# Optimization experiments

Hardware: AMD Instinct MI355X
Metric: run time of the kernel (lower is better)

The kernel has to match this reference:

```python
import jax, jax.numpy as jnp
import numpy as np

N_NODES = 100000
N_REL = 500
DIM = 200
N_EDGES = 200000
T_STEPS = 3
EPS = 1e-12


def _l2norm(x):
    # F.normalize(x): L2 along last dim with eps clamp
    n = jnp.sqrt(jnp.sum(x * x, axis=-1, keepdims=True))
    return x / jnp.maximum(n, EPS)


def _rgcn_layer(h, r, src, rel, dst, W_msg, W_loop):
    # UnionRGCN layer: msg = (h[src] + r[rel]) @ W_msg, mean-aggregated at dst,
    # plus self-loop transform. No activation (active=False), dropout=0.
    msg = (h[src] + r[rel]) @ W_msg                      # [E, D]
    deg = jax.ops.segment_sum(jnp.ones((src.shape[0],), h.dtype), dst,
                              num_segments=N_NODES)       # [N]
    agg = jax.ops.segment_sum(msg, dst, num_segments=N_NODES)
    agg = agg / jnp.maximum(deg, 1.0)[:, None]
    return agg + h @ W_loop


def setup_inputs() -> dict:
    key = jax.random.key(0)
    ks = jax.random.split(key, 10)
    edge_list = []
    for t in range(T_STEPS):
        kt = jax.random.fold_in(ks[0], t)
        k1, k2, k3 = jax.random.split(kt, 3)
        src = jax.random.randint(k1, (N_EDGES,), 0, N_NODES)
        rel = jax.random.randint(k2, (N_EDGES,), 0, N_REL)
        dst = jax.random.randint(k3, (N_EDGES,), 0, N_NODES)
        edge_list.append(jnp.stack([src, rel, dst], axis=1))
    edges = jnp.stack(edge_list)  # [T, E, 3]
    s = 1.0 / np.sqrt(DIM)
    return {
        "edges": edges,
        "entity_embed": jax.random.normal(ks[1], (N_NODES, DIM), jnp.float32),
        "relation_embed": jax.random.normal(ks[2], (N_REL, DIM), jnp.float32),
        "W_msg1": jax.random.normal(ks[3], (DIM, DIM), jnp.float32) * s,
        "W_loop1": jax.random.normal(ks[4], (DIM, DIM), jnp.float32) * s,
        "W_msg2": jax.random.normal(ks[5], (DIM, DIM), jnp.float32) * s,
        "W_loop2": jax.random.normal(ks[6], (DIM, DIM), jnp.float32) * s,
        "time_gate_weight": jax.random.normal(ks[7], (DIM, DIM), jnp.float32) * s * np.sqrt(2.0),
        "time_gate_bias": jnp.zeros((DIM,), jnp.float32),
    }


def reference(edges, entity_embed, relation_embed, W_msg1, W_loop1, W_msg2,
              W_loop2, time_gate_weight, time_gate_bias):
    h = _l2norm(entity_embed)
    r = _l2norm(relation_embed)
    for t in range(T_STEPS):  # small fixed temporal loop, as in source
        src, rel, dst = edges[t, :, 0], edges[t, :, 1], edges[t, :, 2]
        cur = _rgcn_layer(h, r, src, rel, dst, W_msg1, W_loop1)
        cur = _rgcn_layer(cur, r, src, rel, dst, W_msg2, W_loop2)
        cur = _l2norm(cur)
        gate = jax.nn.sigmoid(h @ time_gate_weight + time_gate_bias)
        h = _l2norm(gate * cur + (1.0 - gate) * h)
    return h
```

## Files before the change

kernel.cpp:

```cpp
#include <hip/hip_runtime.h>
#include <math.h>

#define DIMN   200
#define NNODES 100000
#define NREL   500
#define NEDGES 200000
#define TSTEPS 3
#define KSTEPS 7
#define NB16   16
#define WPK_ELEMS (KSTEPS * NB16 * 64 * 8)
#define SCAN_B 1024
#define NBN    6252
#define FRAG_STRIDE 3584

typedef float  v4f  __attribute__((ext_vector_type(4)));
typedef __bf16 v8bf __attribute__((ext_vector_type(8)));

__device__ __forceinline__ size_t frag_chunk(int nb, int c, int r) {
    return (size_t)(nb * KSTEPS + (c >> 2)) * 512 + (size_t)((c & 3) * 128 + r * 8);
}

__launch_bounds__(256)
__global__ void l2norm_pro(const float* __restrict__ in, __bf16* __restrict__ outR,
                           __bf16* __restrict__ outF, int nrows)
{
    int idx  = blockIdx.x * 256 + threadIdx.x;
    int node = idx >> 5;
    int ch   = idx & 31;
    if (node >= nrows) return;
    float v[8] = {};
    if (ch < 25) {
        const float4* p = (const float4*)(in + (size_t)node * DIMN + ch * 8);
        float4 f0 = p[0], f1 = p[1];
        v[0]=f0.x; v[1]=f0.y; v[2]=f0.z; v[3]=f0.w;
        v[4]=f1.x; v[5]=f1.y; v[6]=f1.z; v[7]=f1.w;
    }
    float ss = 0.0f;
    #pragma unroll
    for (int k = 0; k < 8; ++k) ss += v[k] * v[k];
    #pragma unroll
    for (int off = 16; off; off >>= 1) ss += __shfl_xor(ss, off, 64);
    float s = 1.0f / fmaxf(sqrtf(ss), 1e-12f);
    #pragma unroll
    for (int k = 0; k < 8; ++k) v[k] *= s;
    if (ch < 25) {
        v8bf o;
        #pragma unroll
        for (int k = 0; k < 8; ++k) o[k] = (__bf16)v[k];
        *(v8bf*)(outR + (size_t)node * DIMN + ch * 8) = o;
    }
    if (outF && ch < 28) {
        v8bf o;
        #pragma unroll
        for (int k = 0; k < 8; ++k) o[k] = (ch < 25) ? (__bf16)v[k] : (__bf16)0.0f;
        *(v8bf*)(outF + frag_chunk(node >> 4, ch, node & 15)) = o;
    }
}

__launch_bounds__(256)
__global__ void edge_hist3(const int* __restrict__ edges, int* __restrict__ counts)
{
    int e = blockIdx.x * 256 + threadIdx.x;
    if (e < TSTEPS * NEDGES) {
        int t = e / NEDGES;
        atomicAdd(&counts[t * NNODES + edges[(size_t)e * 3 + 2]], 1);
    }
}

__launch_bounds__(SCAN_B)
__global__ void scan1(const int* __restrict__ counts, int* __restrict__ tmp,
                      int* __restrict__ bsum, int n)
{
    __shared__ int sh[SCAN_B];
    int i = blockIdx.x * SCAN_B + threadIdx.x;
    int v = (i < n) ? counts[i] : 0;
    sh[threadIdx.x] = v;
    __syncthreads();
    for (int off = 1; off < SCAN_B; off <<= 1) {
        int t = (threadIdx.x >= off) ? sh[threadIdx.x - off] : 0;
        __syncthreads();
        sh[threadIdx.x] += t;
        __syncthreads();
    }
    if (i < n) tmp[i] = sh[threadIdx.x];
    if (threadIdx.x == SCAN_B - 1) bsum[blockIdx.x] = sh[threadIdx.x];
}

__launch_bounds__(SCAN_B)
__global__ void scan2(int* __restrict__ bsum, int nb)
{
    __shared__ int sh[SCAN_B];
    int v = (threadIdx.x < nb) ? bsum[threadIdx.x] : 0;
    sh[threadIdx.x] = v;
    __syncthreads();
    for (int off = 1; off < SCAN_B; off <<= 1) {
        int t = (threadIdx.x >= off) ? sh[threadIdx.x - off] : 0;
        __syncthreads();
        sh[threadIdx.x] += t;
        __syncthreads();
    }
    if (threadIdx.x < nb) bsum[threadIdx.x] = sh[threadIdx.x] - v;
}

__launch_bounds__(SCAN_B)
__global__ void scan3(const int* __restrict__ tmp, const int* __restrict__ bsum,
                      int* __restrict__ offs, int n)
{
    int i = blockIdx.x * SCAN_B + threadIdx.x;
    if (i < n) offs[i + 1] = tmp[i] + bsum[blockIdx.x];
    if (i == 0) offs[0] = 0;
}

__launch_bounds__(256)
__global__ void edge_fill3(const int* __restrict__ edges, const int* __restrict__ offs,
                           int* __restrict__ cursor, int2* __restrict__ sorted)
{
    int e = blockIdx.x * 256 + threadIdx.x;
    if (e >= TSTEPS * NEDGES) return;
    int t = e / NEDGES;
    int s = edges[(size_t)e * 3 + 0];
    int r = edges[(size_t)e * 3 + 1];
    int d = edges[(size_t)e * 3 + 2];
    int sn = t * NNODES + d;
    int p = offs[sn] + atomicAdd(&cursor[sn], 1);
    sorted[p] = make_int2(s, r);
}

__launch_bounds__(256)
__global__ void agg_S(const int* __restrict__ offs, const int2* __restrict__ sorted,
                      const __bf16* __restrict__ XR, const __bf16* __restrict__ RnR,
                      __bf16* __restrict__ SF, int nnodes)
{
    int wave = (int)((blockIdx.x * blockDim.x + threadIdx.x) >> 6);
    int lane = threadIdx.x & 63;
    if (wave >= nnodes) return;
    int beg = offs[wave], end = offs[wave + 1];
    int ch = lane & 31;
    bool act = ch < 25;

    float acc[8] = {};
    for (int e = beg; e < end; ++e) {
        int2 sr = sorted[e];
        const __bf16* base = (lane < 32) ? (XR + (size_t)sr.x * DIMN)
                                         : (RnR + (size_t)sr.y * DIMN);
        v8bf v = {};
        if (act) v = *(const v8bf*)(base + ch * 8);
        #pragma unroll
        for (int k = 0; k < 8; ++k) acc[k] += (float)v[k];
    }
    #pragma unroll
    for (int k = 0; k < 8; ++k) acc[k] += __shfl_xor(acc[k], 32, 64);

    float rdeg = 1.0f / fmaxf((float)(end - beg), 1.0f);
    if (lane < 32 && ch < 28) {
        v8bf o;
        #pragma unroll
        for (int k = 0; k < 8; ++k) o[k] = act ? (__bf16)(acc[k] * rdeg) : (__bf16)0.0f;
        *(v8bf*)(SF + frag_chunk(wave >> 4, ch, wave & 15)) = o;
    }
}

__launch_bounds__(256)
__global__ void pack_w(const float* __restrict__ W0, const float* __restrict__ W1,
                       const float* __restrict__ W2, const float* __restrict__ W3,
                       const float* __restrict__ W4, __bf16* __restrict__ out)
{
    int id = blockIdx.x * 256 + threadIdx.x;
    const int nchunk = KSTEPS * NB16 * 64;
    if (id >= 5 * nchunk) return;
    int wi = id / nchunk;
    int c  = id % nchunk;
    const float* W = wi == 0 ? W0 : wi == 1 ? W1 : wi == 2 ? W2 : wi == 3 ? W3 : W4;
    int s    = c >> 10;
    int nb   = (c & 1023) >> 6;
    int lane = c & 63;
    int kbase = s * 32 + (lane >> 4) * 8;
    int n     = nb * 16 + (lane & 15);
    __bf16* dst = out + (size_t)wi * WPK_ELEMS + (size_t)c * 8;
    #pragma unroll
    for (int j = 0; j < 8; ++j) {
        int k = kbase + j;
        float v = (k < DIMN && n < DIMN) ? W[k * DIMN + n] : 0.0f;
        dst[j] = (__bf16)v;
    }
}

__launch_bounds__(512)
__global__ void gemm_dual(const __bf16* __restrict__ A1, const __bf16* __restrict__ W1,
                          const __bf16* __restrict__ A2, const __bf16* __restrict__ W2,
                          __bf16* __restrict__ OutR, __bf16* __restrict__ OutF, int M)
{
    const int tid  = threadIdx.x;
    const int w    = tid >> 6;
    const int lane = tid & 63;
    const int rlo  = lane & 15;
    const int g    = lane >> 4;
    const int nb0  = blockIdx.x * 4;
    const int bm   = blockIdx.x * 64;

    __shared__ __bf16 T[64][264];

    v4f acc[4][2];
    #pragma unroll
    for (int mi = 0; mi < 4; ++mi)
        #pragma unroll
        for (int ni = 0; ni < 2; ++ni)
            acc[mi][ni] = (v4f){0.f, 0.f, 0.f, 0.f};

    const __bf16* w1b = W1 + (size_t)(w * 2 * 64 + lane) * 8;
    const __bf16* w2b = W2 + (size_t)(w * 2 * 64 + lane) * 8;

    #pragma unroll
    for (int s = 0; s < KSTEPS; ++s) {
        v8bf b1[2], b2[2];
        #pragma unroll
        for (int ni = 0; ni < 2; ++ni) {
            size_t bo = ((size_t)s * NB16 * 64 + ni * 64) * 8;
            b1[ni] = *(const v8bf*)(w1b + bo);
            b2[ni] = *(const v8bf*)(w2b + bo);
        }
        #pragma unroll
        for (int mi = 0; mi < 4; ++mi) {
            size_t aoff = (size_t)((nb0 + mi) * KSTEPS + s) * 512 + lane * 8;
            v8bf a1 = *(const v8bf*)(A1 + aoff);
            v8bf a2 = *(const v8bf*)(A2 + aoff);
            #pragma unroll
            for (int ni = 0; ni < 2; ++ni)
                acc[mi][ni] = __builtin_amdgcn_mfma_f32_16x16x32_bf16(a1, b1[ni], acc[mi][ni], 0, 0, 0);
            #pragma unroll
            for (int ni = 0; ni < 2; ++ni)
                acc[mi][ni] = __builtin_amdgcn_mfma_f32_16x16x32_bf16(a2, b2[ni], acc[mi][ni], 0, 0, 0);
        }
    }

    #pragma unroll
    for (int mi = 0; mi < 4; ++mi)
        #pragma unroll
        for (int reg = 0; reg < 4; ++reg)
            #pragma unroll
            for (int ni = 0; ni < 2; ++ni)
                T[mi * 16 + g * 4 + reg][w * 32 + ni * 16 + rlo] = (__bf16)acc[mi][ni][reg];
    __syncthreads();

    #pragma unroll
    for (int j = 0; j < 4; ++j) {
        int it = tid + j * 512;
        if (it < 1792) {
            int slot = it & 63;
            int q = it >> 6;
            int s = q % 7, nb = q / 7;
            *(v8bf*)(OutF + (size_t)((nb0 + nb) * KSTEPS + s) * 512 + slot * 8) =
                *(const v8bf*)&T[nb * 16 + (slot & 15)][s * 32 + (slot >> 4) * 8];
        }
    }
    #pragma unroll
    for (int j = 0; j < 4; ++j) {
        int it = tid + j * 512;
        if (it < 1600) {
            int row = it / 25, ch = it - row * 25;
            int gr = bm + row;
            if (gr < M)
                *(v8bf*)(OutR + (size_t)gr * DIMN + ch * 8) = *(const v8bf*)&T[row][ch * 8];
        }
    }
}

__launch_bounds__(512)
__global__ void gemm_mega(const __bf16* __restrict__ A1, const __bf16* __restrict__ W1,
                          const __bf16* __restrict__ A2, const __bf16* __restrict__ W2,
                          const __bf16* __restrict__ A3, const __bf16* __restrict__ W3,
                          const float* __restrict__ Bias,
                          __bf16* __restrict__ HR, __bf16* __restrict__ HF,
                          float* __restrict__ DoutF, int M, int finalStep)
{
    const int tid  = threadIdx.x;
    const int w    = tid >> 6;
    const int lane = tid & 63;
    const int rlo  = lane & 15;
    const int g    = lane >> 4;
    const int nb0  = blockIdx.x * 2;
    const int bm   = blockIdx.x * 32;

    __shared__ __bf16 T[32][264];
    __shared__ float  rsq1[32][8];
    __shared__ float  rsq2[32][8];

    v4f acc1[2][2], acc2[2][2];
    #pragma unroll
    for (int mi = 0; mi < 2; ++mi)
        #pragma unroll
        for (int ni = 0; ni < 2; ++ni) {
            acc1[mi][ni] = (v4f){0.f, 0.f, 0.f, 0.f};
            acc2[mi][ni] = (v4f){0.f, 0.f, 0.f, 0.f};
        }

    const __bf16* w1b = W1 + (size_t)(w * 2 * 64 + lane) * 8;
    const __bf16* w2b = W2 + (size_t)(w * 2 * 64 + lane) * 8;
    const __bf16* w3b = W3 + (size_t)(w * 2 * 64 + lane) * 8;

    for (int s = 0; s < KSTEPS; ++s) {
        v8bf b1[2], b2[2], b3[2];
        #pragma unroll
        for (int ni = 0; ni < 2; ++ni) {
            size_t bo = ((size_t)s * NB16 * 64 + ni * 64) * 8;
            b1[ni] = *(const v8bf*)(w1b + bo);
            b2[ni] = *(const v8bf*)(w2b + bo);
            b3[ni] = *(const v8bf*)(w3b + bo);
        }
        #pragma unroll
        for (int mi = 0; mi < 2; ++mi) {
            size_t aoff = (size_t)((nb0 + mi) * KSTEPS + s) * 512 + lane * 8;
            v8bf a1 = *(const v8bf*)(A1 + aoff);
            v8bf a2 = *(const v8bf*)(A2 + aoff);
            v8bf a3 = *(const v8bf*)(A3 + aoff);
            #pragma unroll
            for (int ni = 0; ni < 2; ++ni)
                acc1[mi][ni] = __builtin_amdgcn_mfma_f32_16x16x32_bf16(a1, b1[ni], acc1[mi][ni], 0, 0, 0);
            #pragma unroll
            for (int ni = 0; ni < 2; ++ni)
                acc1[mi][ni] = __builtin_amdgcn_mfma_f32_16x16x32_bf16(a2, b2[ni], acc1[mi][ni], 0, 0, 0);
            #pragma unroll
            for (int ni = 0; ni < 2; ++ni)
                acc2[mi][ni] = __builtin_amdgcn_mfma_f32_16x16x32_bf16(a3, b3[ni], acc2[mi][ni], 0, 0, 0);
        }
    }

    #pragma unroll
    for (int mi = 0; mi < 2; ++mi)
        #pragma unroll
        for (int reg = 0; reg < 4; ++reg) {
            float ss = 0.0f;
            #pragma unroll
            for (int ni = 0; ni < 2; ++ni) ss += acc1[mi][ni][reg] * acc1[mi][ni][reg];
            ss += __shfl_xor(ss, 1, 64);
            ss += __shfl_xor(ss, 2, 64);
            ss += __shfl_xor(ss, 4, 64);
            ss += __shfl_xor(ss, 8, 64);
            if (rlo == 0) rsq1[mi * 16 + g * 4 + reg][w] = ss;
        }
    #pragma unroll
    for (int j = 0; j < 2; ++j) {
        int it = tid + j * 512;
        if (it < 800) {
            int row = it / 25, ch = it - row * 25;
            int gr = bm + row;
            v8bf hv = {};
            if (gr < M) hv = *(const v8bf*)(HR + (size_t)gr * DIMN + ch * 8);
            *(v8bf*)&T[row][ch * 8] = hv;
        }
    }
    __syncthreads();

    #pragma unroll
    for (int mi = 0; mi < 2; ++mi)
        #pragma unroll
        for (int reg = 0; reg < 4; ++reg) {
            int rl = mi * 16 + g * 4 + reg;
            float tot = rsq1[rl][0] + rsq1[rl][1] + rsq1[rl][2] + rsq1[rl][3]
                      + rsq1[rl][4] + rsq1[rl][5] + rsq1[rl][6] + rsq1[rl][7];
            float sc1 = 1.0f / fmaxf(sqrtf(tot), 1e-12f);
            float ss = 0.0f;
            #pragma unroll
            for (int ni = 0; ni < 2; ++ni) {
                int c = w * 32 + ni * 16 + rlo;
                float v = 0.0f;
                if (c < DIMN) {
                    float cur = acc1[mi][ni][reg] * sc1;
                    float gg  = 1.0f / (1.0f + __expf(-(acc2[mi][ni][reg] + Bias[c])));
                    float hh  = (float)T[rl][c];
                    v = gg * cur + (1.0f - gg) * hh;
                }
                acc1[mi][ni][reg] = v;
                ss += v * v;
            }
            ss += __shfl_xor(ss, 1, 64);
            ss += __shfl_xor(ss, 2, 64);
            ss += __shfl_xor(ss, 4, 64);
            ss += __shfl_xor(ss, 8, 64);
            if (rlo == 0) rsq2[rl][w] = ss;
        }
    __syncthreads();

    #pragma unroll
    for (int mi = 0; mi < 2; ++mi)
        #pragma unroll
        for (int reg = 0; reg < 4; ++reg) {
            int rl = mi * 16 + g * 4 + reg;
            float tot = rsq2[rl][0] + rsq2[rl][1] + rsq2[rl][2] + rsq2[rl][3]
                      + rsq2[rl][4] + rsq2[rl][5] + rsq2[rl][6] + rsq2[rl][7];
            float sc2 = 1.0f / fmaxf(sqrtf(tot), 1e-12f);
            #pragma unroll
            for (int ni = 0; ni < 2; ++ni) {
                int c = w * 32 + ni * 16 + rlo;
                T[rl][c] = (__bf16)(acc1[mi][ni][reg] * sc2);
            }
        }
    __syncthreads();

    if (!finalStep) {
        #pragma unroll
        for (int j = 0; j < 2; ++j) {
            int it = tid + j * 512;
            if (it < 800) {
                int row = it / 25, ch = it - row * 25;
                int gr = bm + row;
                if (gr < M)
                    *(v8bf*)(HR + (size_t)gr * DIMN + ch * 8) = *(const v8bf*)&T[row][ch * 8];
            }
        }
        #pragma unroll
        for (int j = 0; j < 2; ++j) {
            int it = tid + j * 512;
            if (it < 896) {
                int slot = it & 63;
                int q = it >> 6;
                int s = q % 7, nb = q / 7;
                *(v8bf*)(HF + (size_t)((nb0 + nb) * KSTEPS + s) * 512 + slot * 8) =
                    *(const v8bf*)&T[nb * 16 + (slot & 15)][s * 32 + (slot >> 4) * 8];
            }
        }
    } else {
        #pragma unroll
        for (int j = 0; j < 2; ++j) {
            int it = tid + j * 512;
            if (it < 800) {
                int row = it / 25, ch = it - row * 25;
                int gr = bm + row;
                if (gr < M) {
                    v8bf o = *(const v8bf*)&T[row][ch * 8];
                    float4* q0 = (float4*)(DoutF + (size_t)gr * DIMN + ch * 8);
                    q0[0] = make_float4((float)o[0], (float)o[1], (float)o[2], (float)o[3]);
                    q0[1] = make_float4((float)o[4], (float)o[5], (float)o[6], (float)o[7]);
                }
            }
        }
    }
}

extern "C" void kernel_launch(void* const* d_in, const int* in_sizes, int n_in,
                              void* d_out, int out_size, void* d_ws, size_t ws_size,
                              hipStream_t stream)
{
    const int*   edges = (const int*)  d_in[0];
    const float* ent   = (const float*)d_in[1];
    const float* relE  = (const float*)d_in[2];
    const float* Wm1   = (const float*)d_in[3];
    const float* Wl1   = (const float*)d_in[4];
    const float* Wm2   = (const float*)d_in[5];
    const float* Wl2   = (const float*)d_in[6];
    const float* Wtg   = (const float*)d_in[7];
    const float* bias  = (const float*)d_in[8];
    float* Dout = (float*)d_out;

    const size_t NM    = (size_t)NNODES * DIMN;
    const size_t FRAGN = (size_t)NBN * FRAG_STRIDE;

    __bf16* hR   = (__bf16*)d_ws;
    __bf16* hF   = hR + NM;
    __bf16* SF   = hF + FRAGN;
    __bf16* BR   = SF + FRAGN;
    __bf16* BF   = BR + NM;
    __bf16* RnR  = BF + FRAGN;
    __bf16* Wpk  = RnR + (size_t)NREL * DIMN;
    __bf16* pWm1 = Wpk + 0 * (size_t)WPK_ELEMS;
    __bf16* pWl1 = Wpk + 1 * (size_t)WPK_ELEMS;
    __bf16* pWm2 = Wpk + 2 * (size_t)WPK_ELEMS;
    __bf16* pWl2 = Wpk + 3 * (size_t)WPK_ELEMS;
    __bf16* pWtg = Wpk + 4 * (size_t)WPK_ELEMS;
    int*  counts = (int*)(Wpk + 5 * (size_t)WPK_ELEMS);
    int*  cursor = counts + TSTEPS * NNODES;
    int2* sorted = (int2*)(cursor + TSTEPS * NNODES);
    int*  offs   = (int*)(sorted + TSTEPS * NEDGES);
    int*  bsum   = offs + (TSTEPS * NNODES + 1);
    int*  stmp   = bsum + SCAN_B;

    dim3 blk(256);
    const int GD = (NNODES + 63) / 64;
    const int GM = (NNODES + 31) / 32;
    dim3 ngrid32((NNODES * 32 + 255) / 256);
    dim3 rgrid32((NREL * 32 + 255) / 256);
    dim3 agrid((NNODES + 3) / 4);
    dim3 egrid3((TSTEPS * NEDGES + 255) / 256);
    const int NTOT = TSTEPS * NNODES;
    const int NSB  = (NTOT + SCAN_B - 1) / SCAN_B;

    pack_w<<<dim3((5 * KSTEPS * NB16 * 64 + 255) / 256), blk, 0, stream>>>(Wm1, Wl1, Wm2, Wl2, Wtg, Wpk);
    l2norm_pro<<<ngrid32, blk, 0, stream>>>(ent, hR, hF, NNODES);
    l2norm_pro<<<rgrid32, blk, 0, stream>>>(relE, RnR, nullptr, NREL);

    hipMemsetAsync(counts, 0, 2 * NTOT * sizeof(int), stream);
    edge_hist3<<<egrid3, blk, 0, stream>>>(edges, counts);
    scan1<<<NSB, SCAN_B, 0, stream>>>(counts, stmp, bsum, NTOT);
    scan2<<<1, SCAN_B, 0, stream>>>(bsum, NSB);
    scan3<<<NSB, SCAN_B, 0, stream>>>(stmp, bsum, offs, NTOT);
    edge_fill3<<<egrid3, blk, 0, stream>>>(edges, offs, cursor, sorted);

    for (int t = 0; t < 3; ++t) {
        const int* offsT = offs + (size_t)t * NNODES;
        agg_S<<<agrid, blk, 0, stream>>>(offsT, sorted, hR, RnR, SF, NNODES);
        gemm_dual<<<GD, dim3(512), 0, stream>>>(SF, pWm1, hF, pWl1, BR, BF, NNODES);
        agg_S<<<agrid, blk, 0, stream>>>(offsT, sorted, BR, RnR, SF, NNODES);
        gemm_mega<<<GM, dim3(512), 0, stream>>>(SF, pWm2, BF, pWl2, hF, pWtg, bias,
                                                hR, hF, Dout, NNODES, (t == 2) ? 1 : 0);
    }
}
```

Measured before the change: 967.3 us.

## Replace dual row/fragment buffers with single padded row-major bf16 layout

Activations were kept in two copies, a row-major buffer for gathers and an MFMA fragment-packed buffer for GEMMs. They now use one row-major buffer padded to a stride of 224. The GEMMs read A operands directly with per-row pointers, and the weight packing is reordered so each lane's K steps are contiguous. This removes the duplicate fragment writes in every producer kernel and shrinks the workspace. In exchange the GEMM A loads are less coalesced than the fragment-contiguous layout, and the gathers read a padded stride.

```diff
diff --git a/kernel.cpp b/kernel.cpp
--- a/kernel.cpp
+++ b/kernel.cpp
@@ -1,28 +1,23 @@
 #include <hip/hip_runtime.h>
 #include <math.h>
 
-#define DIMN   200
-#define NNODES 100000
-#define NREL   500
-#define NEDGES 200000
-#define TSTEPS 3
-#define KSTEPS 7
-#define NB16   16
+#define DIMN    200
+#define RSTRIDE 224
+#define NNODES  100000
+#define NREL    500
+#define NEDGES  200000
+#define TSTEPS  3
+#define KSTEPS  7
+#define NB16    16
 #define WPK_ELEMS (KSTEPS * NB16 * 64 * 8)
-#define SCAN_B 1024
-#define NBN    6252
-#define FRAG_STRIDE 3584
+#define SCAN_B  1024
 
 typedef float  v4f  __attribute__((ext_vector_type(4)));
 typedef __bf16 v8bf __attribute__((ext_vector_type(8)));
 
-__device__ __forceinline__ size_t frag_chunk(int nb, int c, int r) {
-    return (size_t)(nb * KSTEPS + (c >> 2)) * 512 + (size_t)((c & 3) * 128 + r * 8);
-}
 
 __launch_bounds__(256)
-__global__ void l2norm_pro(const float* __restrict__ in, __bf16* __restrict__ outR,
-                           __bf16* __restrict__ outF, int nrows)
+__global__ void l2norm_pro(const float* __restrict__ in, __bf16* __restrict__ out, int nrows)
 {
     int idx  = blockIdx.x * 256 + threadIdx.x;
     int node = idx >> 5;
@@ -41,19 +36,11 @@
     #pragma unroll
     for (int off = 16; off; off >>= 1) ss += __shfl_xor(ss, off, 64);
     float s = 1.0f / fmaxf(sqrtf(ss), 1e-12f);
-    #pragma unroll
-    for (int k = 0; k < 8; ++k) v[k] *= s;
-    if (ch < 25) {
+    if (ch < 28) {
         v8bf o;
         #pragma unroll
-        for (int k = 0; k < 8; ++k) o[k] = (__bf16)v[k];
-        *(v8bf*)(outR + (size_t)node * DIMN + ch * 8) = o;
-    }
-    if (outF && ch < 28) {
-        v8bf o;
-        #pragma unroll
-        for (int k = 0; k < 8; ++k) o[k] = (ch < 25) ? (__bf16)v[k] : (__bf16)0.0f;
-        *(v8bf*)(outF + frag_chunk(node >> 4, ch, node & 15)) = o;
+        for (int k = 0; k < 8; ++k) o[k] = (ch < 25) ? (__bf16)(v[k] * s) : (__bf16)0.0f;
+        *(v8bf*)(out + (size_t)node * RSTRIDE + ch * 8) = o;
     }
 }
 
@@ -129,7 +116,7 @@
 __launch_bounds__(256)
 __global__ void agg_S(const int* __restrict__ offs, const int2* __restrict__ sorted,
                       const __bf16* __restrict__ XR, const __bf16* __restrict__ RnR,
-                      __bf16* __restrict__ SF, int nnodes)
+                      __bf16* __restrict__ SR, int nnodes)
 {
     int wave = (int)((blockIdx.x * blockDim.x + threadIdx.x) >> 6);
     int lane = threadIdx.x & 63;
@@ -141,8 +128,8 @@
     float acc[8] = {};
     for (int e = beg; e < end; ++e) {
         int2 sr = sorted[e];
-        const __bf16* base = (lane < 32) ? (XR + (size_t)sr.x * DIMN)
-                                         : (RnR + (size_t)sr.y * DIMN);
+        const __bf16* base = (lane < 32) ? (XR + (size_t)sr.x * RSTRIDE)
+                                         : (RnR + (size_t)sr.y * RSTRIDE);
         v8bf v = {};
         if (act) v = *(const v8bf*)(base + ch * 8);
         #pragma unroll
@@ -156,7 +143,7 @@
         v8bf o;
         #pragma unroll
         for (int k = 0; k < 8; ++k) o[k] = act ? (__bf16)(acc[k] * rdeg) : (__bf16)0.0f;
-        *(v8bf*)(SF + frag_chunk(wave >> 4, ch, wave & 15)) = o;
+        *(v8bf*)(SR + (size_t)wave * RSTRIDE + ch * 8) = o;
     }
 }
 
@@ -171,9 +158,10 @@
     int wi = id / nchunk;
     int c  = id % nchunk;
     const float* W = wi == 0 ? W0 : wi == 1 ? W1 : wi == 2 ? W2 : wi == 3 ? W3 : W4;
-    int s    = c >> 10;
-    int nb   = (c & 1023) >> 6;
-    int lane = c & 63;
+    int nb   = c / 448;
+    int rem  = c - nb * 448;
+    int lane = rem / 7;
+    int s    = rem - lane * 7;
     int kbase = s * 32 + (lane >> 4) * 8;
     int n     = nb * 16 + (lane & 15);
     __bf16* dst = out + (size_t)wi * WPK_ELEMS + (size_t)c * 8;
@@ -188,14 +176,13 @@
 __launch_bounds__(512)
 __global__ void gemm_dual(const __bf16* __restrict__ A1, const __bf16* __restrict__ W1,
                           const __bf16* __restrict__ A2, const __bf16* __restrict__ W2,
-                          __bf16* __restrict__ OutR, __bf16* __restrict__ OutF, int M)
+                          __bf16* __restrict__ OutR, int M)
 {
     const int tid  = threadIdx.x;
     const int w    = tid >> 6;
     const int lane = tid & 63;
     const int rlo  = lane & 15;
-    const int g    = lane >> 4;
-    const int nb0  = blockIdx.x * 4;
+    const int g8   = lane >> 4;
     const int bm   = blockIdx.x * 64;
 
     __shared__ __bf16 T[64][264];
@@ -207,23 +194,36 @@
         for (int ni = 0; ni < 2; ++ni)
             acc[mi][ni] = (v4f){0.f, 0.f, 0.f, 0.f};
 
-    const __bf16* w1b = W1 + (size_t)(w * 2 * 64 + lane) * 8;
-    const __bf16* w2b = W2 + (size_t)(w * 2 * 64 + lane) * 8;
+    const __bf16* a1p[4];
+    const __bf16* a2p[4];
+    #pragma unroll
+    for (int mi = 0; mi < 4; ++mi) {
+        int rr = bm + mi * 16 + rlo;
+        if (rr >= M) rr = M - 1;
+        a1p[mi] = A1 + (size_t)rr * RSTRIDE + g8 * 8;
+        a2p[mi] = A2 + (size_t)rr * RSTRIDE + g8 * 8;
+    }
+    const __bf16* b1p[2];
+    const __bf16* b2p[2];
+    #pragma unroll
+    for (int ni = 0; ni < 2; ++ni) {
+        size_t bo = ((size_t)(w * 2 + ni) * 448 + lane * 7) * 8;
+        b1p[ni] = W1 + bo;
+        b2p[ni] = W2 + bo;
+    }
 
     #pragma unroll
     for (int s = 0; s < KSTEPS; ++s) {
         v8bf b1[2], b2[2];
         #pragma unroll
         for (int ni = 0; ni < 2; ++ni) {
-            size_t bo = ((size_t)s * NB16 * 64 + ni * 64) * 8;
-            b1[ni] = *(const v8bf*)(w1b + bo);
-            b2[ni] = *(const v8bf*)(w2b + bo);
+            b1[ni] = *(const v8bf*)(b1p[ni] + s * 8);
+            b2[ni] = *(const v8bf*)(b2p[ni] + s * 8);
         }
         #pragma unroll
         for (int mi = 0; mi < 4; ++mi) {
-            size_t aoff = (size_t)((nb0 + mi) * KSTEPS + s) * 512 + lane * 8;
-            v8bf a1 = *(const v8bf*)(A1 + aoff);
-            v8bf a2 = *(const v8bf*)(A2 + aoff);
+            v8bf a1 = *(const v8bf*)(a1p[mi] + s * 32);
+            v8bf a2 = *(const v8bf*)(a2p[mi] + s * 32);
             #pragma unroll
             for (int ni = 0; ni < 2; ++ni)
                 acc[mi][ni] = __builtin_amdgcn_mfma_f32_16x16x32_bf16(a1, b1[ni], acc[mi][ni], 0, 0, 0);
@@ -239,28 +239,17 @@
         for (int reg = 0; reg < 4; ++reg)
             #pragma unroll
             for (int ni = 0; ni < 2; ++ni)
-                T[mi * 16 + g * 4 + reg][w * 32 + ni * 16 + rlo] = (__bf16)acc[mi][ni][reg];
+                T[mi * 16 + g8 * 4 + reg][w * 32 + ni * 16 + rlo] = (__bf16)acc[mi][ni][reg];
     __syncthreads();
 
     #pragma unroll
     for (int j = 0; j < 4; ++j) {
         int it = tid + j * 512;
         if (it < 1792) {
-            int slot = it & 63;
-            int q = it >> 6;
-            int s = q % 7, nb = q / 7;
-            *(v8bf*)(OutF + (size_t)((nb0 + nb) * KSTEPS + s) * 512 + slot * 8) =
-                *(const v8bf*)&T[nb * 16 + (slot & 15)][s * 32 + (slot >> 4) * 8];
-        }
-    }
-    #pragma unroll
-    for (int j = 0; j < 4; ++j) {
-        int it = tid + j * 512;
-        if (it < 1600) {
-            int row = it / 25, ch = it - row * 25;
+            int row = it / 28, ch = it - row * 28;
             int gr = bm + row;
             if (gr < M)
-                *(v8bf*)(OutR + (size_t)gr * DIMN + ch * 8) = *(const v8bf*)&T[row][ch * 8];
+                *(v8bf*)(OutR + (size_t)gr * RSTRIDE + ch * 8) = *(const v8bf*)&T[row][ch * 8];
         }
     }
 }
@@ -268,17 +257,15 @@
 __launch_bounds__(512)
 __global__ void gemm_mega(const __bf16* __restrict__ A1, const __bf16* __restrict__ W1,
                           const __bf16* __restrict__ A2, const __bf16* __restrict__ W2,
-                          const __bf16* __restrict__ A3, const __bf16* __restrict__ W3,
+                          __bf16* __restrict__ HR, const __bf16* __restrict__ W3,
                           const float* __restrict__ Bias,
-                          __bf16* __restrict__ HR, __bf16* __restrict__ HF,
                           float* __restrict__ DoutF, int M, int finalStep)
 {
     const int tid  = threadIdx.x;
     const int w    = tid >> 6;
     const int lane = tid & 63;
     const int rlo  = lane & 15;
-    const int g    = lane >> 4;
-    const int nb0  = blockIdx.x * 2;
+    const int g8   = lane >> 4;
     const int bm   = blockIdx.x * 32;
 
     __shared__ __bf16 T[32][264];
@@ -294,25 +281,42 @@
             acc2[mi][ni] = (v4f){0.f, 0.f, 0.f, 0.f};
         }
 
-    const __bf16* w1b = W1 + (size_t)(w * 2 * 64 + lane) * 8;
-    const __bf16* w2b = W2 + (size_t)(w * 2 * 64 + lane) * 8;
-    const __bf16* w3b = W3 + (size_t)(w * 2 * 64 + lane) * 8;
-
+    const __bf16* a1p[2];
+    const __bf16* a2p[2];
+    const __bf16* a3p[2];
+    #pragma unroll
+    for (int mi = 0; mi < 2; ++mi) {
+        int rr = bm + mi * 16 + rlo;
+        if (rr >= M) rr = M - 1;
+        a1p[mi] = A1 + (size_t)rr * RSTRIDE + g8 * 8;
+        a2p[mi] = A2 + (size_t)rr * RSTRIDE + g8 * 8;
+        a3p[mi] = HR + (size_t)rr * RSTRIDE + g8 * 8;
+    }
+    const __bf16* b1p[2];
+    const __bf16* b2p[2];
+    const __bf16* b3p[2];
+    #pragma unroll
+    for (int ni = 0; ni < 2; ++ni) {
+        size_t bo = ((size_t)(w * 2 + ni) * 448 + lane * 7) * 8;
+        b1p[ni] = W1 + bo;
+        b2p[ni] = W2 + bo;
+        b3p[ni] = W3 + bo;
+    }
+
+    #pragma unroll
     for (int s = 0; s < KSTEPS; ++s) {
         v8bf b1[2], b2[2], b3[2];
         #pragma unroll
         for (int ni = 0; ni < 2; ++ni) {
-            size_t bo = ((size_t)s * NB16 * 64 + ni * 64) * 8;
-            b1[ni] = *(const v8bf*)(w1b + bo);
-            b2[ni] = *(const v8bf*)(w2b + bo);
-            b3[ni] = *(const v8bf*)(w3b + bo);
+            b1[ni] = *(const v8bf*)(b1p[ni] + s * 8);
+            b2[ni] = *(const v8bf*)(b2p[ni] + s * 8);
+            b3[ni] = *(const v8bf*)(b3p[ni] + s * 8);
         }
         #pragma unroll
         for (int mi = 0; mi < 2; ++mi) {
-            size_t aoff = (size_t)((nb0 + mi) * KSTEPS + s) * 512 + lane * 8;
-            v8bf a1 = *(const v8bf*)(A1 + aoff);
-            v8bf a2 = *(const v8bf*)(A2 + aoff);
-            v8bf a3 = *(const v8bf*)(A3 + aoff);
+            v8bf a1 = *(const v8bf*)(a1p[mi] + s * 32);
+            v8bf a2 = *(const v8bf*)(a2p[mi] + s * 32);
+            v8bf a3 = *(const v8bf*)(a3p[mi] + s * 32);
             #pragma unroll
             for (int ni = 0; ni < 2; ++ni)
                 acc1[mi][ni] = __builtin_amdgcn_mfma_f32_16x16x32_bf16(a1, b1[ni], acc1[mi][ni], 0, 0, 0);
@@ -336,7 +340,7 @@
             ss += __shfl_xor(ss, 2, 64);
             ss += __shfl_xor(ss, 4, 64);
             ss += __shfl_xor(ss, 8, 64);
-            if (rlo == 0) rsq1[mi * 16 + g * 4 + reg][w] = ss;
+            if (rlo == 0) rsq1[mi * 16 + g8 * 4 + reg][w] = ss;
         }
     #pragma unroll
     for (int j = 0; j < 2; ++j) {
@@ -345,7 +349,7 @@
             int row = it / 25, ch = it - row * 25;
             int gr = bm + row;
             v8bf hv = {};
-            if (gr < M) hv = *(const v8bf*)(HR + (size_t)gr * DIMN + ch * 8);
+            if (gr < M) hv = *(const v8bf*)(HR + (size_t)gr * RSTRIDE + ch * 8);
             *(v8bf*)&T[row][ch * 8] = hv;
         }
     }
@@ -355,7 +359,7 @@
     for (int mi = 0; mi < 2; ++mi)
         #pragma unroll
         for (int reg = 0; reg < 4; ++reg) {
-            int rl = mi * 16 + g * 4 + reg;
+            int rl = mi * 16 + g8 * 4 + reg;
             float tot = rsq1[rl][0] + rsq1[rl][1] + rsq1[rl][2] + rsq1[rl][3]
                       + rsq1[rl][4] + rsq1[rl][5] + rsq1[rl][6] + rsq1[rl][7];
             float sc1 = 1.0f / fmaxf(sqrtf(tot), 1e-12f);
@@ -385,7 +389,7 @@
     for (int mi = 0; mi < 2; ++mi)
         #pragma unroll
         for (int reg = 0; reg < 4; ++reg) {
-            int rl = mi * 16 + g * 4 + reg;
+            int rl = mi * 16 + g8 * 4 + reg;
             float tot = rsq2[rl][0] + rsq2[rl][1] + rsq2[rl][2] + rsq2[rl][3]
                       + rsq2[rl][4] + rsq2[rl][5] + rsq2[rl][6] + rsq2[rl][7];
             float sc2 = 1.0f / fmaxf(sqrtf(tot), 1e-12f);
@@ -401,22 +405,11 @@
         #pragma unroll
         for (int j = 0; j < 2; ++j) {
             int it = tid + j * 512;
-            if (it < 800) {
-                int row = it / 25, ch = it - row * 25;
+            if (it < 896) {
+                int row = it / 28, ch = it - row * 28;
                 int gr = bm + row;
                 if (gr < M)
-                    *(v8bf*)(HR + (size_t)gr * DIMN + ch * 8) = *(const v8bf*)&T[row][ch * 8];
-            }
-        }
-        #pragma unroll
-        for (int j = 0; j < 2; ++j) {
-            int it = tid + j * 512;
-            if (it < 896) {
-                int slot = it & 63;
-                int q = it >> 6;
-                int s = q % 7, nb = q / 7;
-                *(v8bf*)(HF + (size_t)((nb0 + nb) * KSTEPS + s) * 512 + slot * 8) =
-                    *(const v8bf*)&T[nb * 16 + (slot & 15)][s * 32 + (slot >> 4) * 8];
+                    *(v8bf*)(HR + (size_t)gr * RSTRIDE + ch * 8) = *(const v8bf*)&T[row][ch * 8];
             }
         }
     } else {
@@ -452,16 +445,13 @@
     const float* bias  = (const float*)d_in[8];
     float* Dout = (float*)d_out;
 
-    const size_t NM    = (size_t)NNODES * DIMN;
-    const size_t FRAGN = (size_t)NBN * FRAG_STRIDE;
+    const size_t NM2 = (size_t)NNODES * RSTRIDE;
 
     __bf16* hR   = (__bf16*)d_ws;
-    __bf16* hF   = hR + NM;
-    __bf16* SF   = hF + FRAGN;
-    __bf16* BR   = SF + FRAGN;
-    __bf16* BF   = BR + NM;
-    __bf16* RnR  = BF + FRAGN;
-    __bf16* Wpk  = RnR + (size_t)NREL * DIMN;
+    __bf16* SR   = hR + NM2;
+    __bf16* BR   = SR + NM2;
+    __bf16* RnR  = BR + NM2;
+    __bf16* Wpk  = RnR + (size_t)NREL * RSTRIDE;
     __bf16* pWm1 = Wpk + 0 * (size_t)WPK_ELEMS;
     __bf16* pWl1 = Wpk + 1 * (size_t)WPK_ELEMS;
     __bf16* pWm2 = Wpk + 2 * (size_t)WPK_ELEMS;
@@ -485,8 +475,8 @@
     const int NSB  = (NTOT + SCAN_B - 1) / SCAN_B;
 
     pack_w<<<dim3((5 * KSTEPS * NB16 * 64 + 255) / 256), blk, 0, stream>>>(Wm1, Wl1, Wm2, Wl2, Wtg, Wpk);
-    l2norm_pro<<<ngrid32, blk, 0, stream>>>(ent, hR, hF, NNODES);
-    l2norm_pro<<<rgrid32, blk, 0, stream>>>(relE, RnR, nullptr, NREL);
+    l2norm_pro<<<ngrid32, blk, 0, stream>>>(ent, hR, NNODES);
+    l2norm_pro<<<rgrid32, blk, 0, stream>>>(relE, RnR, NREL);
 
     hipMemsetAsync(counts, 0, 2 * NTOT * sizeof(int), stream);
     edge_hist3<<<egrid3, blk, 0, stream>>>(edges, counts);
@@ -497,10 +487,10 @@
 
     for (int t = 0; t < 3; ++t) {
         const int* offsT = offs + (size_t)t * NNODES;
-        agg_S<<<agrid, blk, 0, stream>>>(offsT, sorted, hR, RnR, SF, NNODES);
-        gemm_dual<<<GD, dim3(512), 0, stream>>>(SF, pWm1, hF, pWl1, BR, BF, NNODES);
-        agg_S<<<agrid, blk, 0, stream>>>(offsT, sorted, BR, RnR, SF, NNODES);
-        gemm_mega<<<GM, dim3(512), 0, stream>>>(SF, pWm2, BF, pWl2, hF, pWtg, bias,
-                                                hR, hF, Dout, NNODES, (t == 2) ? 1 : 0);
-    }
-}
+        agg_S<<<agrid, blk, 0, stream>>>(offsT, sorted, hR, RnR, SR, NNODES);
+        gemm_dual<<<GD, dim3(512), 0, stream>>>(SR, pWm1, hR, pWl1, BR, NNODES);
+        agg_S<<<agrid, blk, 0, stream>>>(offsT, sorted, BR, RnR, SR, NNODES);
+        gemm_mega<<<GM, dim3(512), 0, stream>>>(SR, pWm2, BR, pWl2, hR, pWtg, bias,
+                                                Dout, NNODES, (t == 2) ? 1 : 0);
+    }
+}
```

Result: slower. 1.633 ms (+68.8%).
